# Optimization experiments

Hardware: AMD Instinct MI355X
Metric: run time of the kernel (lower is better)

Reference implementation:

```python
import jax, jax.numpy as jnp
import numpy as np

D = 128          # feature / hidden dim
K = 3            # SortPooling k (hard-coded in Topkpool)
NUM_CLASS = 10
EPS = 1e-5       # BatchNorm eps


def setup_inputs() -> dict:
    key = jax.random.key(0)
    ks = jax.random.split(key, 24)
    G, NPG = 512, 200
    N = G * NPG
    E = 1638400
    inp = {
        "x": jax.random.normal(ks[0], (N, D), jnp.float32),
        "src": jax.random.randint(ks[1], (E,), 0, N),
        "dst": jax.random.randint(ks[2], (E,), 0, N),
        "num_graphs": G,
        "nodes_per_graph": NPG,
    }
    s = 1.0 / np.sqrt(D)
    for i in (1, 2, 3):
        inp[f"W{i}"] = jax.random.uniform(ks[2 + i], (D, D), jnp.float32, -s, s)
        inp[f"b{i}"] = jnp.zeros((D,), jnp.float32)
        inp[f"g{i}"] = jnp.ones((D,), jnp.float32)   # BN gamma
        inp[f"bt{i}"] = jnp.zeros((D,), jnp.float32)  # BN beta
    sp = 1.0 / np.sqrt(K * D)
    for i in range(4):
        inp[f"P{i}w"] = jax.random.uniform(ks[10 + i], (K * D, NUM_CLASS), jnp.float32, -sp, sp)
        inp[f"P{i}b"] = jnp.zeros((NUM_CLASS,), jnp.float32)
    return inp


def _graph_conv(h, src, dst, W, b, n):
    # DGL GraphConv, norm='both': D_in^{-1/2} A (D_out^{-1/2} h) W + b
    one = jnp.ones((src.shape[0],), h.dtype)
    deg_out = jnp.zeros((n,), h.dtype).at[src].add(one)
    deg_in = jnp.zeros((n,), h.dtype).at[dst].add(one)
    h = h * jax.lax.rsqrt(jnp.maximum(deg_out, 1.0))[:, None]
    agg = jax.ops.segment_sum(h[src], dst, num_segments=n)  # [N, D] scatter-add
    agg = agg * jax.lax.rsqrt(jnp.maximum(deg_in, 1.0))[:, None]
    return agg @ W + b


def _bn_relu(h, g, bt):
    mu = h.mean(axis=0)
    var = jnp.mean((h - mu) ** 2, axis=0)  # biased var, torch BN training mode
    return jax.nn.relu((h - mu) * jax.lax.rsqrt(var + EPS) * g + bt)


def _sort_pool(h, G, npg):
    # DGL SortPooling: sort each node's feature vector ascending, then pick
    # top-K nodes per graph by last (max) channel, concatenate features.
    d = h.shape[-1]
    hs = jnp.sort(h, axis=-1).reshape(G, npg, d)
    idx = jax.lax.top_k(hs[:, :, -1], K)[1]                       # [G, K]
    return jnp.take_along_axis(hs, idx[:, :, None], axis=1).reshape(G, K * d)


def reference(x, W1, b1, g1, bt1, W2, b2, g2, bt2, W3, b3, g3, bt3,
              P0w, P0b, P1w, P1b, P2w, P2b, P3w, P3b,
              src, dst, num_graphs, nodes_per_graph):
    n = x.shape[0]
    reps = [x]
    h = x
    for W, b, g, bt in ((W1, b1, g1, bt1), (W2, b2, g2, bt2), (W3, b3, g3, bt3)):
        h = _bn_relu(_graph_conv(h, src, dst, W, b, n), g, bt)
        reps.append(h)
    score = jnp.zeros((num_graphs, NUM_CLASS), x.dtype)
    for h_i, Pw, Pb in zip(reps, (P0w, P1w, P2w, P3w), (P0b, P1b, P2b, P3b)):
        score = score + _sort_pool(h_i, num_graphs, nodes_per_graph) @ Pw + Pb
    return score
```

## Files before the change

### kernel.cpp

```cpp
#include <hip/hip_runtime.h>
#include <hip/hip_bf16.h>

#define D 128
#define KTOP 3
#define NCLS 10
#define EPS 1e-5f
#define GBM 128


__global__ void deg_kernel(const int* __restrict__ src, const int* __restrict__ dst,
                           int* __restrict__ deg_out, int* __restrict__ deg_in, int E) {
    int e = blockIdx.x * blockDim.x + threadIdx.x;
    if (e >= E) return;
    atomicAdd(&deg_out[src[e]], 1);
    atomicAdd(&deg_in[dst[e]], 1);
}

__global__ void rs_kernel(const int* __restrict__ deg_out, const int* __restrict__ deg_in,
                          float* __restrict__ rs_out, float* __restrict__ rs_in, int N) {
    int i = blockIdx.x * blockDim.x + threadIdx.x;
    if (i >= N) return;
    int a = deg_out[i]; if (a < 1) a = 1;
    int b = deg_in[i];  if (b < 1) b = 1;
    rs_out[i] = rsqrtf((float)a);
    rs_in[i]  = rsqrtf((float)b);
}


__global__ __launch_bounds__(1024) void scan_partial(const int* __restrict__ deg,
                                                     int* __restrict__ bsum, int N) {
    __shared__ int red[1024];
    int t = threadIdx.x;
    int i = blockIdx.x * 1024 + t;
    red[t] = (i < N) ? deg[i] : 0;
    __syncthreads();
    for (int s = 512; s > 0; s >>= 1) {
        if (t < s) red[t] += red[t + s];
        __syncthreads();
    }
    if (t == 0) bsum[blockIdx.x] = red[0];
}

__global__ __launch_bounds__(1024) void scan_bsum(const int* __restrict__ bsum,
                                                  int* __restrict__ bbase, int nb) {
    __shared__ int sh[1024];
    int t = threadIdx.x;
    sh[t] = (t < nb) ? bsum[t] : 0;
    __syncthreads();
    for (int off = 1; off < 1024; off <<= 1) {
        int v = (t >= off) ? sh[t - off] : 0;
        __syncthreads();
        sh[t] += v;
        __syncthreads();
    }
    if (t < nb) bbase[t] = (t == 0) ? 0 : sh[t - 1];
}

__global__ __launch_bounds__(1024) void scan_final(const int* __restrict__ deg,
                                                   const int* __restrict__ bbase,
                                                   int* __restrict__ offs, int N) {
    __shared__ int sh[1024];
    int t = threadIdx.x;
    int i = blockIdx.x * 1024 + t;
    int v = (i < N) ? deg[i] : 0;
    sh[t] = v;
    __syncthreads();
    for (int off = 1; off < 1024; off <<= 1) {
        int u = (t >= off) ? sh[t - off] : 0;
        __syncthreads();
        sh[t] += u;
        __syncthreads();
    }
    int excl = bbase[blockIdx.x] + sh[t] - v;
    if (i < N) offs[i] = excl;
    if (i == N - 1) offs[N] = excl + v;
}

__global__ void csr_scatter(const int* __restrict__ src, const int* __restrict__ dst,
                            const float* __restrict__ rs_out,
                            const int* __restrict__ offs, int* __restrict__ cursor,
                            int2* __restrict__ csrw, int E) {
    int e = blockIdx.x * blockDim.x + threadIdx.x;
    if (e >= E) return;
    int d = dst[e], s = src[e];
    int pos = offs[d] + atomicAdd(&cursor[d], 1);
    int2 p; p.x = s; p.y = __float_as_int(rs_out[s]);
    csrw[pos] = p;
}


__global__ __launch_bounds__(256) void aggregate_kernel(const float* __restrict__ hin,
        const int* __restrict__ offs, const int2* __restrict__ csrw,
        const float* __restrict__ rs_in, float* __restrict__ hout, int N) {
    int node = (blockIdx.x * 256 + threadIdx.x) >> 5;
    int l = threadIdx.x & 31;
    if (node >= N) return;
    int beg = offs[node], end = offs[node + 1];
    const float* base = hin + 4 * l;
    float ax0=0.f, ay0=0.f, az0=0.f, aw0=0.f;
    float ax1=0.f, ay1=0.f, az1=0.f, aw1=0.f;
    float ax2=0.f, ay2=0.f, az2=0.f, aw2=0.f;
    float ax3=0.f, ay3=0.f, az3=0.f, aw3=0.f;
    int nq = (end - beg) >> 2;
    int e = beg;
    int2 c0, c1, c2, c3;
    if (nq) { c0 = csrw[e]; c1 = csrw[e+1]; c2 = csrw[e+2]; c3 = csrw[e+3]; }
    for (int q = 0; q < nq; ++q) {
        int2 n0 = c0, n1 = c1, n2 = c2, n3 = c3;
        int en = e + 4;
        if (q + 1 < nq) { n0 = csrw[en]; n1 = csrw[en+1]; n2 = csrw[en+2]; n3 = csrw[en+3]; }
        float4 v0 = *reinterpret_cast<const float4*>(base + (size_t)c0.x * D);
        float4 v1 = *reinterpret_cast<const float4*>(base + (size_t)c1.x * D);
        float4 v2 = *reinterpret_cast<const float4*>(base + (size_t)c2.x * D);
        float4 v3 = *reinterpret_cast<const float4*>(base + (size_t)c3.x * D);
        float w0 = __int_as_float(c0.y), w1 = __int_as_float(c1.y);
        float w2 = __int_as_float(c2.y), w3 = __int_as_float(c3.y);
        ax0 += w0*v0.x; ay0 += w0*v0.y; az0 += w0*v0.z; aw0 += w0*v0.w;
        ax1 += w1*v1.x; ay1 += w1*v1.y; az1 += w1*v1.z; aw1 += w1*v1.w;
        ax2 += w2*v2.x; ay2 += w2*v2.y; az2 += w2*v2.z; aw2 += w2*v2.w;
        ax3 += w3*v3.x; ay3 += w3*v3.y; az3 += w3*v3.z; aw3 += w3*v3.w;
        c0 = n0; c1 = n1; c2 = n2; c3 = n3;
        e = en;
    }
    for (; e < end; ++e) {
        int2 c = csrw[e];
        float w = __int_as_float(c.y);
        float4 v = *reinterpret_cast<const float4*>(base + (size_t)c.x * D);
        ax0 += w*v.x; ay0 += w*v.y; az0 += w*v.z; aw0 += w*v.w;
    }
    float ri = rs_in[node];
    float4 r;
    r.x = ((ax0 + ax1) + (ax2 + ax3)) * ri;
    r.y = ((ay0 + ay1) + (ay2 + ay3)) * ri;
    r.z = ((az0 + az1) + (az2 + az3)) * ri;
    r.w = ((aw0 + aw1) + (aw2 + aw3)) * ri;
    *reinterpret_cast<float4*>(hout + (size_t)node * D + 4 * l) = r;
}


__global__ __launch_bounds__(512) void gemm_bn(const float* __restrict__ ain,
        const float* __restrict__ W, const float* __restrict__ bias,
        float* __restrict__ hout, float* __restrict__ bnsums, int N) {
    __shared__ __align__(16) float Wl[64][D];
    int t = threadIdx.x;
    int cg = t & 15;
    int rs = t >> 4;
    int c0 = cg * 8;
    size_t rowBase = (size_t)blockIdx.x * GBM + 4 * rs;

    float acc[4][8];
#pragma unroll
    for (int i = 0; i < 4; ++i)
#pragma unroll
        for (int j = 0; j < 8; ++j) acc[i][j] = 0.f;

    for (int kc = 0; kc < D; kc += 64) {
        __syncthreads();
        const float4* Wv = reinterpret_cast<const float4*>(W + (size_t)kc * D);
        float4* Wd = reinterpret_cast<float4*>(&Wl[0][0]);
#pragma unroll
        for (int i = 0; i < 4; ++i) Wd[t + 512 * i] = Wv[t + 512 * i];
        __syncthreads();
#pragma unroll 2
        for (int k4 = 0; k4 < 16; ++k4) {
            const float* ap = ain + rowBase * D + kc + 4 * k4;
            float4 a0 = *reinterpret_cast<const float4*>(ap);
            float4 a1 = *reinterpret_cast<const float4*>(ap + D);
            float4 a2 = *reinterpret_cast<const float4*>(ap + 2 * D);
            float4 a3 = *reinterpret_cast<const float4*>(ap + 3 * D);
#pragma unroll
            for (int j = 0; j < 4; ++j) {
                int kk = 4 * k4 + j;
                float4 w0 = *reinterpret_cast<const float4*>(&Wl[kk][c0]);
                float4 w1 = *reinterpret_cast<const float4*>(&Wl[kk][c0 + 4]);
                float av[4];
                av[0] = (j==0)?a0.x:(j==1)?a0.y:(j==2)?a0.z:a0.w;
                av[1] = (j==0)?a1.x:(j==1)?a1.y:(j==2)?a1.z:a1.w;
                av[2] = (j==0)?a2.x:(j==1)?a2.y:(j==2)?a2.z:a2.w;
                av[3] = (j==0)?a3.x:(j==1)?a3.y:(j==2)?a3.z:a3.w;
                float wv[8] = {w0.x, w0.y, w0.z, w0.w, w1.x, w1.y, w1.z, w1.w};
#pragma unroll
                for (int i = 0; i < 4; ++i)
#pragma unroll
                    for (int jj = 0; jj < 8; ++jj) acc[i][jj] += av[i] * wv[jj];
            }
        }
    }

    float4 b0 = *reinterpret_cast<const float4*>(&bias[c0]);
    float4 b1 = *reinterpret_cast<const float4*>(&bias[c0 + 4]);
    float bv[8] = {b0.x, b0.y, b0.z, b0.w, b1.x, b1.y, b1.z, b1.w};
    float cs[8], cq[8];
#pragma unroll
    for (int j = 0; j < 8; ++j) { cs[j] = 0.f; cq[j] = 0.f; }
#pragma unroll
    for (int i = 0; i < 4; ++i) {
#pragma unroll
        for (int j = 0; j < 8; ++j) {
            float v = acc[i][j] + bv[j];
            acc[i][j] = v;
            cs[j] += v;
            cq[j] += v * v;
        }
    }
#pragma unroll
    for (int i = 0; i < 4; ++i) {
        size_t row = rowBase + i;
        float4 o0, o1;
        o0.x = acc[i][0]; o0.y = acc[i][1]; o0.z = acc[i][2]; o0.w = acc[i][3];
        o1.x = acc[i][4]; o1.y = acc[i][5]; o1.z = acc[i][6]; o1.w = acc[i][7];
        *reinterpret_cast<float4*>(&hout[row * D + c0])     = o0;
        *reinterpret_cast<float4*>(&hout[row * D + c0 + 4]) = o1;
    }
#pragma unroll
    for (int j = 0; j < 8; ++j) {
        cs[j] += __shfl_xor(cs[j], 16, 64); cq[j] += __shfl_xor(cq[j], 16, 64);
        cs[j] += __shfl_xor(cs[j], 32, 64); cq[j] += __shfl_xor(cq[j], 32, 64);
    }
    __syncthreads();
    float* red = &Wl[0][0];
    int wid = t >> 6, lane = t & 63;
    if (lane < 16) {
#pragma unroll
        for (int j = 0; j < 8; ++j) {
            red[wid * 256 + lane * 16 + j]     = cs[j];
            red[wid * 256 + lane * 16 + 8 + j] = cq[j];
        }
    }
    __syncthreads();
    if (t < 256) {
        float s = 0.f;
#pragma unroll
        for (int w = 0; w < 8; ++w) s += red[w * 256 + t];
        int cgi = t >> 4, r = t & 15;
        int ch = cgi * 8 + (r & 7);
        atomicAdd(&bnsums[(r < 8 ? 0 : D) + ch], s);
    }
}


__global__ void bn_final(const float* __restrict__ sums, const float* __restrict__ g,
                         const float* __restrict__ bt, float* __restrict__ sc,
                         float* __restrict__ sh, int N) {
    int c = threadIdx.x;
    if (c >= D) return;
    float mu  = sums[c] / (float)N;
    float var = sums[D + c] / (float)N - mu * mu;
    float inv = rsqrtf(var + EPS);
    float scale = g[c] * inv;
    sc[c] = scale;
    sh[c] = bt[c] - mu * scale;
}

__global__ __launch_bounds__(256) void bn_apply_relu_max(float* __restrict__ h,
        const float* __restrict__ sc, const float* __restrict__ sh,
        float* __restrict__ nodemax, int N) {
    int node = (blockIdx.x * 256 + threadIdx.x) >> 5;
    int l = threadIdx.x & 31;
    if (node >= N) return;
    float4 v = *reinterpret_cast<const float4*>(h + (size_t)node * D + 4 * l);
    float4 a = *reinterpret_cast<const float4*>(sc + 4 * l);
    float4 b = *reinterpret_cast<const float4*>(sh + 4 * l);
    v.x = fmaxf(fmaf(v.x, a.x, b.x), 0.f);
    v.y = fmaxf(fmaf(v.y, a.y, b.y), 0.f);
    v.z = fmaxf(fmaf(v.z, a.z, b.z), 0.f);
    v.w = fmaxf(fmaf(v.w, a.w, b.w), 0.f);
    *reinterpret_cast<float4*>(h + (size_t)node * D + 4 * l) = v;
    float m = fmaxf(fmaxf(v.x, v.y), fmaxf(v.z, v.w));
#pragma unroll
    for (int d = 16; d > 0; d >>= 1) m = fmaxf(m, __shfl_xor(m, d, 64));
    if (l == 0) nodemax[node] = m;
}

__global__ __launch_bounds__(256) void rowmax_kernel(const float* __restrict__ h,
                                                     float* __restrict__ nodemax, int N) {
    int node = (blockIdx.x * 256 + threadIdx.x) >> 5;
    int l = threadIdx.x & 31;
    if (node >= N) return;
    float4 v = *reinterpret_cast<const float4*>(h + (size_t)node * D + 4 * l);
    float m = fmaxf(fmaxf(v.x, v.y), fmaxf(v.z, v.w));
#pragma unroll
    for (int d = 16; d > 0; d >>= 1) m = fmaxf(m, __shfl_xor(m, d, 64));
    if (l == 0) nodemax[node] = m;
}


__global__ __launch_bounds__(256) void topk_kernel(const float* __restrict__ nodemax,
                                                   int* __restrict__ tk, int NPG) {
    int g = blockIdx.x;
    int t = threadIdx.x;
    __shared__ float ov[256];
    __shared__ float sv[256];
    __shared__ int   si[256];
    ov[t] = (t < NPG) ? nodemax[(size_t)g * NPG + t] : -3.4e38f;
    __syncthreads();
    for (int sel = 0; sel < 3; ++sel) {
        sv[t] = ov[t]; si[t] = t;
        __syncthreads();
        for (int s = 128; s > 0; s >>= 1) {
            if (t < s) {
                float a = sv[t], b = sv[t + s];
                int ia = si[t], ib = si[t + s];
                if (b > a || (b == a && ib < ia)) { sv[t] = b; si[t] = ib; }
            }
            __syncthreads();
        }
        if (t == 0) {
            tk[g * 3 + sel] = g * NPG + si[0];
            ov[si[0]] = -3.4e38f;
        }
        __syncthreads();
    }
}

__global__ void score_init(float* __restrict__ score, const float* __restrict__ b0,
                           const float* __restrict__ b1, const float* __restrict__ b2,
                           const float* __restrict__ b3, int G) {
    int i = blockIdx.x * blockDim.x + threadIdx.x;
    if (i >= G * NCLS) return;
    int c = i % NCLS;
    score[i] = b0[c] + b1[c] + b2[c] + b3[c];
}

__global__ __launch_bounds__(128) void sort_head(const float* __restrict__ h,
        const int* __restrict__ tk, const float* __restrict__ Pw,
        float* __restrict__ score, int G) {
    int b = blockIdx.x;
    int g = b / KTOP, k = b - g * KTOP;
    int node = tk[b];
    int t = threadIdx.x;
    __shared__ float s[D];
    __shared__ float red[2][NCLS];
    s[t] = h[(size_t)node * D + t];
    __syncthreads();
    for (int size = 2; size <= D; size <<= 1) {
        for (int stride = size >> 1; stride > 0; stride >>= 1) {
            int ixj = t ^ stride;
            if (ixj > t) {
                float a = s[t], c = s[ixj];
                bool up = ((t & size) == 0);
                if ((a > c) == up) { s[t] = c; s[ixj] = a; }
            }
            __syncthreads();
        }
    }
    float v = s[t];
    const float* pw = Pw + (size_t)(k * D + t) * NCLS;
    float part[NCLS];
#pragma unroll
    for (int c = 0; c < NCLS; ++c) part[c] = v * pw[c];
    int lane = t & 63, wid = t >> 6;
#pragma unroll
    for (int c = 0; c < NCLS; ++c) {
        float x = part[c];
#pragma unroll
        for (int o = 32; o > 0; o >>= 1) x += __shfl_down(x, o, 64);
        if (lane == 0) red[wid][c] = x;
    }
    __syncthreads();
    if (t < NCLS) atomicAdd(&score[g * NCLS + t], red[0][t] + red[1][t]);
}


extern "C" void kernel_launch(void* const* d_in, const int* in_sizes, int n_in,
                              void* d_out, int out_size, void* d_ws, size_t ws_size,
                              hipStream_t stream) {
    const float* x   = (const float*)d_in[0];
    const int*   src = (const int*)d_in[1];
    const int*   dst = (const int*)d_in[2];
    const float* W[3]  = {(const float*)d_in[5],  (const float*)d_in[9],  (const float*)d_in[13]};
    const float* bb[3] = {(const float*)d_in[6],  (const float*)d_in[10], (const float*)d_in[14]};
    const float* gg[3] = {(const float*)d_in[7],  (const float*)d_in[11], (const float*)d_in[15]};
    const float* bt[3] = {(const float*)d_in[8],  (const float*)d_in[12], (const float*)d_in[16]};
    const float* Pw[4] = {(const float*)d_in[17], (const float*)d_in[19], (const float*)d_in[21], (const float*)d_in[23]};
    const float* Pb[4] = {(const float*)d_in[18], (const float*)d_in[20], (const float*)d_in[22], (const float*)d_in[24]};

    int N = in_sizes[0] / D;
    int E = in_sizes[1];
    int G = out_size / NCLS;
    int NPG = N / G;
    float* score = (float*)d_out;

    size_t NF = (size_t)N * D;
    float* fws     = (float*)d_ws;
    float* H       = fws;
    float* T       = H + NF;
    float* rs_out  = T + NF;
    float* rs_in   = rs_out + N;
    float* nodemax = rs_in + N;
    float* bnsums  = nodemax + N;
    float* bscale  = bnsums + 6 * D;
    float* bshift  = bscale + D;
    int* deg_out = (int*)(bshift + D);
    int* deg_in  = deg_out + N;
    int* cursor  = deg_in + N;
    int* offs    = cursor + N;
    int* bsum    = offs + N + 2;
    int* bbase   = bsum + 1024;
    int2* csrw   = (int2*)(bbase + 1024);
    int* tk      = (int*)(csrw + E);

    int nb = (N + 1023) >> 10;

    hipMemsetAsync(deg_out, 0, sizeof(int) * (size_t)3 * N, stream);
    hipMemsetAsync(bnsums, 0, sizeof(float) * 6 * D, stream);
    deg_kernel<<<(E + 255) / 256, 256, 0, stream>>>(src, dst, deg_out, deg_in, E);
    rs_kernel<<<(N + 255) / 256, 256, 0, stream>>>(deg_out, deg_in, rs_out, rs_in, N);
    scan_partial<<<nb, 1024, 0, stream>>>(deg_in, bsum, N);
    scan_bsum<<<1, 1024, 0, stream>>>(bsum, bbase, nb);
    scan_final<<<nb, 1024, 0, stream>>>(deg_in, bbase, offs, N);
    csr_scatter<<<(E + 255) / 256, 256, 0, stream>>>(src, dst, rs_out, offs, cursor, csrw, E);

    score_init<<<(G * NCLS + 255) / 256, 256, 0, stream>>>(score, Pb[0], Pb[1], Pb[2], Pb[3], G);

    rowmax_kernel<<<N / 8, 256, 0, stream>>>(x, nodemax, N);
    topk_kernel<<<G, 256, 0, stream>>>(nodemax, tk, NPG);
    sort_head<<<G * KTOP, D, 0, stream>>>(x, tk, Pw[0], score, G);

    const float* hin = x;
    for (int l = 0; l < 3; ++l) {
        float* bns = bnsums + l * 2 * D;
        aggregate_kernel<<<N / 8, 256, 0, stream>>>(hin, offs, csrw, rs_in, T, N);
        gemm_bn<<<N / GBM, 512, 0, stream>>>(T, W[l], bb[l], H, bns, N);
        bn_final<<<1, D, 0, stream>>>(bns, gg[l], bt[l], bscale, bshift, N);
        bn_apply_relu_max<<<N / 8, 256, 0, stream>>>(H, bscale, bshift, nodemax, N);
        topk_kernel<<<G, 256, 0, stream>>>(nodemax, tk, NPG);
        sort_head<<<G * KTOP, D, 0, stream>>>(H, tk, Pw[l + 1], score, G);
        hin = H;
    }
}
```

Measured before the change: 887.9 us.

## Pad CSR rows to multiples of eight, fuse prologue kernels, prefetch GEMM weights

CSR row lengths are padded to multiples of 8 with zero-weight entries, so the aggregation loop can read neighbour entries as int4 pairs and process eight neighbours per iteration with no remainder loop. Degree counting, row-max of x and score init are merged into one prologue kernel, and the rsqrt normalisation is folded into the scan. The GEMM prefetches the second weight chunk into registers while the first chunk is computed. In exchange the CSR buffer grows and needs an extra memset, and padded entries still cost gathers of node 0.

```diff
diff --git a/kernel.cpp b/kernel.cpp
--- a/kernel.cpp
+++ b/kernel.cpp
@@ -8,31 +8,56 @@
 #define GBM 128
 
 
-__global__ void deg_kernel(const int* __restrict__ src, const int* __restrict__ dst,
-                           int* __restrict__ deg_out, int* __restrict__ deg_in, int E) {
-    int e = blockIdx.x * blockDim.x + threadIdx.x;
-    if (e >= E) return;
-    atomicAdd(&deg_out[src[e]], 1);
-    atomicAdd(&deg_in[dst[e]], 1);
-}
-
-__global__ void rs_kernel(const int* __restrict__ deg_out, const int* __restrict__ deg_in,
-                          float* __restrict__ rs_out, float* __restrict__ rs_in, int N) {
-    int i = blockIdx.x * blockDim.x + threadIdx.x;
-    if (i >= N) return;
-    int a = deg_out[i]; if (a < 1) a = 1;
-    int b = deg_in[i];  if (b < 1) b = 1;
-    rs_out[i] = rsqrtf((float)a);
-    rs_in[i]  = rsqrtf((float)b);
-}
-
-
-__global__ __launch_bounds__(1024) void scan_partial(const int* __restrict__ deg,
-                                                     int* __restrict__ bsum, int N) {
+__global__ __launch_bounds__(256) void prologue_kernel(
+        const int* __restrict__ src, const int* __restrict__ dst,
+        int* __restrict__ deg_out, int* __restrict__ deg_in, int E,
+        const float* __restrict__ x, float* __restrict__ nodemax, int N,
+        float* __restrict__ score, const float* __restrict__ pb0,
+        const float* __restrict__ pb1, const float* __restrict__ pb2,
+        const float* __restrict__ pb3, int G) {
+    int b = blockIdx.x;
+    int nbDeg = (E + 255) >> 8;
+    if (b < nbDeg) {
+        int e = b * 256 + threadIdx.x;
+        if (e < E) {
+            atomicAdd(&deg_out[src[e]], 1);
+            atomicAdd(&deg_in[dst[e]], 1);
+        }
+        return;
+    }
+    b -= nbDeg;
+    int nbR = N >> 3;
+    if (b < nbR) {
+        int node = b * 8 + (threadIdx.x >> 5);
+        int l = threadIdx.x & 31;
+        float4 v = *reinterpret_cast<const float4*>(x + (size_t)node * D + 4 * l);
+        float m = fmaxf(fmaxf(v.x, v.y), fmaxf(v.z, v.w));
+#pragma unroll
+        for (int d = 16; d > 0; d >>= 1) m = fmaxf(m, __shfl_xor(m, d, 64));
+        if (l == 0) nodemax[node] = m;
+        return;
+    }
+    for (int i = threadIdx.x; i < G * NCLS; i += 256) {
+        int c = i % NCLS;
+        score[i] = pb0[c] + pb1[c] + pb2[c] + pb3[c];
+    }
+}
+
+
+__global__ __launch_bounds__(1024) void scan_partial_rs(const int* __restrict__ deg_in,
+        const int* __restrict__ deg_out, int* __restrict__ bsum,
+        float* __restrict__ rs_in, float* __restrict__ rs_out, int N) {
     __shared__ int red[1024];
     int t = threadIdx.x;
     int i = blockIdx.x * 1024 + t;
-    red[t] = (i < N) ? deg[i] : 0;
+    int dv = 0;
+    if (i < N) {
+        int di = deg_in[i], dox = deg_out[i];
+        rs_in[i]  = rsqrtf((float)(di  < 1 ? 1 : di));
+        rs_out[i] = rsqrtf((float)(dox < 1 ? 1 : dox));
+        dv = (di + 7) & ~7;
+    }
+    red[t] = dv;
     __syncthreads();
     for (int s = 512; s > 0; s >>= 1) {
         if (t < s) red[t] += red[t + s];
@@ -62,7 +87,7 @@
     __shared__ int sh[1024];
     int t = threadIdx.x;
     int i = blockIdx.x * 1024 + t;
-    int v = (i < N) ? deg[i] : 0;
+    int v = (i < N) ? ((deg[i] + 7) & ~7) : 0;
     sh[t] = v;
     __syncthreads();
     for (int off = 1; off < 1024; off <<= 1) {
@@ -97,46 +122,68 @@
     if (node >= N) return;
     int beg = offs[node], end = offs[node + 1];
     const float* base = hin + 4 * l;
-    float ax0=0.f, ay0=0.f, az0=0.f, aw0=0.f;
-    float ax1=0.f, ay1=0.f, az1=0.f, aw1=0.f;
-    float ax2=0.f, ay2=0.f, az2=0.f, aw2=0.f;
-    float ax3=0.f, ay3=0.f, az3=0.f, aw3=0.f;
-    int nq = (end - beg) >> 2;
-    int e = beg;
-    int2 c0, c1, c2, c3;
-    if (nq) { c0 = csrw[e]; c1 = csrw[e+1]; c2 = csrw[e+2]; c3 = csrw[e+3]; }
-    for (int q = 0; q < nq; ++q) {
-        int2 n0 = c0, n1 = c1, n2 = c2, n3 = c3;
-        int en = e + 4;
-        if (q + 1 < nq) { n0 = csrw[en]; n1 = csrw[en+1]; n2 = csrw[en+2]; n3 = csrw[en+3]; }
-        float4 v0 = *reinterpret_cast<const float4*>(base + (size_t)c0.x * D);
-        float4 v1 = *reinterpret_cast<const float4*>(base + (size_t)c1.x * D);
-        float4 v2 = *reinterpret_cast<const float4*>(base + (size_t)c2.x * D);
-        float4 v3 = *reinterpret_cast<const float4*>(base + (size_t)c3.x * D);
-        float w0 = __int_as_float(c0.y), w1 = __int_as_float(c1.y);
-        float w2 = __int_as_float(c2.y), w3 = __int_as_float(c3.y);
-        ax0 += w0*v0.x; ay0 += w0*v0.y; az0 += w0*v0.z; aw0 += w0*v0.w;
-        ax1 += w1*v1.x; ay1 += w1*v1.y; az1 += w1*v1.z; aw1 += w1*v1.w;
-        ax2 += w2*v2.x; ay2 += w2*v2.y; az2 += w2*v2.z; aw2 += w2*v2.w;
-        ax3 += w3*v3.x; ay3 += w3*v3.y; az3 += w3*v3.z; aw3 += w3*v3.w;
-        c0 = n0; c1 = n1; c2 = n2; c3 = n3;
-        e = en;
-    }
-    for (; e < end; ++e) {
-        int2 c = csrw[e];
-        float w = __int_as_float(c.y);
-        float4 v = *reinterpret_cast<const float4*>(base + (size_t)c.x * D);
-        ax0 += w*v.x; ay0 += w*v.y; az0 += w*v.z; aw0 += w*v.w;
+    float4 a0 = {0.f, 0.f, 0.f, 0.f}, a1 = a0;
+    for (int e = beg; e < end; e += 8) {
+        const int4* ce = reinterpret_cast<const int4*>(csrw + e);
+        int4 p0 = ce[0], p1 = ce[1], p2 = ce[2], p3 = ce[3];
+        float4 v0 = *reinterpret_cast<const float4*>(base + (size_t)p0.x * D);
+        float4 v1 = *reinterpret_cast<const float4*>(base + (size_t)p0.z * D);
+        float4 v2 = *reinterpret_cast<const float4*>(base + (size_t)p1.x * D);
+        float4 v3 = *reinterpret_cast<const float4*>(base + (size_t)p1.z * D);
+        float4 v4 = *reinterpret_cast<const float4*>(base + (size_t)p2.x * D);
+        float4 v5 = *reinterpret_cast<const float4*>(base + (size_t)p2.z * D);
+        float4 v6 = *reinterpret_cast<const float4*>(base + (size_t)p3.x * D);
+        float4 v7 = *reinterpret_cast<const float4*>(base + (size_t)p3.z * D);
+        float w0 = __int_as_float(p0.y), w1 = __int_as_float(p0.w);
+        float w2 = __int_as_float(p1.y), w3 = __int_as_float(p1.w);
+        float w4 = __int_as_float(p2.y), w5 = __int_as_float(p2.w);
+        float w6 = __int_as_float(p3.y), w7 = __int_as_float(p3.w);
+        a0.x += w0*v0.x; a0.y += w0*v0.y; a0.z += w0*v0.z; a0.w += w0*v0.w;
+        a1.x += w1*v1.x; a1.y += w1*v1.y; a1.z += w1*v1.z; a1.w += w1*v1.w;
+        a0.x += w2*v2.x; a0.y += w2*v2.y; a0.z += w2*v2.z; a0.w += w2*v2.w;
+        a1.x += w3*v3.x; a1.y += w3*v3.y; a1.z += w3*v3.z; a1.w += w3*v3.w;
+        a0.x += w4*v4.x; a0.y += w4*v4.y; a0.z += w4*v4.z; a0.w += w4*v4.w;
+        a1.x += w5*v5.x; a1.y += w5*v5.y; a1.z += w5*v5.z; a1.w += w5*v5.w;
+        a0.x += w6*v6.x; a0.y += w6*v6.y; a0.z += w6*v6.z; a0.w += w6*v6.w;
+        a1.x += w7*v7.x; a1.y += w7*v7.y; a1.z += w7*v7.z; a1.w += w7*v7.w;
     }
     float ri = rs_in[node];
     float4 r;
-    r.x = ((ax0 + ax1) + (ax2 + ax3)) * ri;
-    r.y = ((ay0 + ay1) + (ay2 + ay3)) * ri;
-    r.z = ((az0 + az1) + (az2 + az3)) * ri;
-    r.w = ((aw0 + aw1) + (aw2 + aw3)) * ri;
+    r.x = (a0.x + a1.x) * ri;
+    r.y = (a0.y + a1.y) * ri;
+    r.z = (a0.z + a1.z) * ri;
+    r.w = (a0.w + a1.w) * ri;
     *reinterpret_cast<float4*>(hout + (size_t)node * D + 4 * l) = r;
 }
 
+
+__device__ __forceinline__ void gemm_chunk(const float* __restrict__ ain, size_t rowBase,
+        int kc, int c0, const float (*Wl)[D], float (&acc)[4][8]) {
+#pragma unroll 2
+    for (int k4 = 0; k4 < 16; ++k4) {
+        const float* ap = ain + rowBase * D + kc + 4 * k4;
+        float4 a0 = *reinterpret_cast<const float4*>(ap);
+        float4 a1 = *reinterpret_cast<const float4*>(ap + D);
+        float4 a2 = *reinterpret_cast<const float4*>(ap + 2 * D);
+        float4 a3 = *reinterpret_cast<const float4*>(ap + 3 * D);
+#pragma unroll
+        for (int j = 0; j < 4; ++j) {
+            int kk = 4 * k4 + j;
+            float4 w0 = *reinterpret_cast<const float4*>(&Wl[kk][c0]);
+            float4 w1 = *reinterpret_cast<const float4*>(&Wl[kk][c0 + 4]);
+            float av[4];
+            av[0] = (j==0)?a0.x:(j==1)?a0.y:(j==2)?a0.z:a0.w;
+            av[1] = (j==0)?a1.x:(j==1)?a1.y:(j==2)?a1.z:a1.w;
+            av[2] = (j==0)?a2.x:(j==1)?a2.y:(j==2)?a2.z:a2.w;
+            av[3] = (j==0)?a3.x:(j==1)?a3.y:(j==2)?a3.z:a3.w;
+            float wv[8] = {w0.x, w0.y, w0.z, w0.w, w1.x, w1.y, w1.z, w1.w};
+#pragma unroll
+            for (int i = 0; i < 4; ++i)
+#pragma unroll
+                for (int jj = 0; jj < 8; ++jj) acc[i][jj] += av[i] * wv[jj];
+        }
+    }
+}
 
 __global__ __launch_bounds__(512) void gemm_bn(const float* __restrict__ ain,
         const float* __restrict__ W, const float* __restrict__ bias,
@@ -154,38 +201,22 @@
 #pragma unroll
         for (int j = 0; j < 8; ++j) acc[i][j] = 0.f;
 
-    for (int kc = 0; kc < D; kc += 64) {
-        __syncthreads();
-        const float4* Wv = reinterpret_cast<const float4*>(W + (size_t)kc * D);
-        float4* Wd = reinterpret_cast<float4*>(&Wl[0][0]);
-#pragma unroll
-        for (int i = 0; i < 4; ++i) Wd[t + 512 * i] = Wv[t + 512 * i];
-        __syncthreads();
-#pragma unroll 2
-        for (int k4 = 0; k4 < 16; ++k4) {
-            const float* ap = ain + rowBase * D + kc + 4 * k4;
-            float4 a0 = *reinterpret_cast<const float4*>(ap);
-            float4 a1 = *reinterpret_cast<const float4*>(ap + D);
-            float4 a2 = *reinterpret_cast<const float4*>(ap + 2 * D);
-            float4 a3 = *reinterpret_cast<const float4*>(ap + 3 * D);
-#pragma unroll
-            for (int j = 0; j < 4; ++j) {
-                int kk = 4 * k4 + j;
-                float4 w0 = *reinterpret_cast<const float4*>(&Wl[kk][c0]);
-                float4 w1 = *reinterpret_cast<const float4*>(&Wl[kk][c0 + 4]);
-                float av[4];
-                av[0] = (j==0)?a0.x:(j==1)?a0.y:(j==2)?a0.z:a0.w;
-                av[1] = (j==0)?a1.x:(j==1)?a1.y:(j==2)?a1.z:a1.w;
-                av[2] = (j==0)?a2.x:(j==1)?a2.y:(j==2)?a2.z:a2.w;
-                av[3] = (j==0)?a3.x:(j==1)?a3.y:(j==2)?a3.z:a3.w;
-                float wv[8] = {w0.x, w0.y, w0.z, w0.w, w1.x, w1.y, w1.z, w1.w};
-#pragma unroll
-                for (int i = 0; i < 4; ++i)
-#pragma unroll
-                    for (int jj = 0; jj < 8; ++jj) acc[i][jj] += av[i] * wv[jj];
-            }
-        }
-    }
+    const float4* Wv = reinterpret_cast<const float4*>(W);
+    float4* Wd = reinterpret_cast<float4*>(&Wl[0][0]);
+    float4 wpre[4];
+#pragma unroll
+    for (int i = 0; i < 4; ++i) wpre[i] = Wv[t + 512 * i];
+#pragma unroll
+    for (int i = 0; i < 4; ++i) Wd[t + 512 * i] = wpre[i];
+#pragma unroll
+    for (int i = 0; i < 4; ++i) wpre[i] = Wv[2048 + t + 512 * i];
+    __syncthreads();
+    gemm_chunk(ain, rowBase, 0, c0, Wl, acc);
+    __syncthreads();
+#pragma unroll
+    for (int i = 0; i < 4; ++i) Wd[t + 512 * i] = wpre[i];
+    __syncthreads();
+    gemm_chunk(ain, rowBase, 64, c0, Wl, acc);
 
     float4 b0 = *reinterpret_cast<const float4*>(&bias[c0]);
     float4 b1 = *reinterpret_cast<const float4*>(&bias[c0 + 4]);
@@ -272,18 +303,6 @@
     if (l == 0) nodemax[node] = m;
 }
 
-__global__ __launch_bounds__(256) void rowmax_kernel(const float* __restrict__ h,
-                                                     float* __restrict__ nodemax, int N) {
-    int node = (blockIdx.x * 256 + threadIdx.x) >> 5;
-    int l = threadIdx.x & 31;
-    if (node >= N) return;
-    float4 v = *reinterpret_cast<const float4*>(h + (size_t)node * D + 4 * l);
-    float m = fmaxf(fmaxf(v.x, v.y), fmaxf(v.z, v.w));
-#pragma unroll
-    for (int d = 16; d > 0; d >>= 1) m = fmaxf(m, __shfl_xor(m, d, 64));
-    if (l == 0) nodemax[node] = m;
-}
-
 
 __global__ __launch_bounds__(256) void topk_kernel(const float* __restrict__ nodemax,
                                                    int* __restrict__ tk, int NPG) {
@@ -311,15 +330,6 @@
         }
         __syncthreads();
     }
-}
-
-__global__ void score_init(float* __restrict__ score, const float* __restrict__ b0,
-                           const float* __restrict__ b1, const float* __restrict__ b2,
-                           const float* __restrict__ b3, int G) {
-    int i = blockIdx.x * blockDim.x + threadIdx.x;
-    if (i >= G * NCLS) return;
-    int c = i % NCLS;
-    score[i] = b0[c] + b1[c] + b2[c] + b3[c];
 }
 
 __global__ __launch_bounds__(128) void sort_head(const float* __restrict__ h,
@@ -382,6 +392,7 @@
     float* score = (float*)d_out;
 
     size_t NF = (size_t)N * D;
+    size_t Epad = (size_t)E + 7 * (size_t)N;
     float* fws     = (float*)d_ws;
     float* H       = fws;
     float* T       = H + NF;
@@ -398,22 +409,24 @@
     int* bsum    = offs + N + 2;
     int* bbase   = bsum + 1024;
     int2* csrw   = (int2*)(bbase + 1024);
-    int* tk      = (int*)(csrw + E);
+    int* tk      = (int*)(csrw + Epad);
 
     int nb = (N + 1023) >> 10;
+    int nbDeg = (E + 255) >> 8;
+    int nbR = N >> 3;
 
     hipMemsetAsync(deg_out, 0, sizeof(int) * (size_t)3 * N, stream);
     hipMemsetAsync(bnsums, 0, sizeof(float) * 6 * D, stream);
-    deg_kernel<<<(E + 255) / 256, 256, 0, stream>>>(src, dst, deg_out, deg_in, E);
-    rs_kernel<<<(N + 255) / 256, 256, 0, stream>>>(deg_out, deg_in, rs_out, rs_in, N);
-    scan_partial<<<nb, 1024, 0, stream>>>(deg_in, bsum, N);
+    hipMemsetAsync(csrw, 0, sizeof(int2) * Epad, stream);
+
+    prologue_kernel<<<nbDeg + nbR + 1, 256, 0, stream>>>(
+        src, dst, deg_out, deg_in, E, x, nodemax, N,
+        score, Pb[0], Pb[1], Pb[2], Pb[3], G);
+    scan_partial_rs<<<nb, 1024, 0, stream>>>(deg_in, deg_out, bsum, rs_in, rs_out, N);
     scan_bsum<<<1, 1024, 0, stream>>>(bsum, bbase, nb);
     scan_final<<<nb, 1024, 0, stream>>>(deg_in, bbase, offs, N);
     csr_scatter<<<(E + 255) / 256, 256, 0, stream>>>(src, dst, rs_out, offs, cursor, csrw, E);
 
-    score_init<<<(G * NCLS + 255) / 256, 256, 0, stream>>>(score, Pb[0], Pb[1], Pb[2], Pb[3], G);
-
-    rowmax_kernel<<<N / 8, 256, 0, stream>>>(x, nodemax, N);
     topk_kernel<<<G, 256, 0, stream>>>(nodemax, tk, NPG);
     sort_head<<<G * KTOP, D, 0, stream>>>(x, tk, Pw[0], score, G);
 
```

Measured after the change: 913.9 us. +2.9%, slower.
